# Kernel tuning notes

Measured on AMD Instinct MI355X. Metric: run time of the kernel, lower is better.

## Reference

```python
import jax, jax.numpy as jnp
import numpy as np

N, H, E, T = 100000, 128, 500000, 6  # nodes, hidden, max edges, edge types


def setup_inputs() -> dict:
    key = jax.random.key(0)
    ks = jax.random.split(key, 16)
    xav_e = float(np.sqrt(6.0 / (H + T * H)))  # xavier_uniform for edge_dense
    xav_h = float(np.sqrt(6.0 / (H + H)))
    u = lambda k, s, a: jax.random.uniform(k, s, jnp.float32, -a, a)
    return {
        "node_embeddings": jax.random.normal(ks[0], (N, H), jnp.float32),
        "W_edge": u(ks[1], (H, T * H), xav_e),
        "b_edge": 1e-6 * jax.random.normal(ks[2], (T * H,), jnp.float32),
        "W_ir": u(ks[3], (H, H), xav_h), "b_ir": jnp.zeros((H,), jnp.float32),
        "W_iz": u(ks[4], (H, H), xav_h), "b_iz": jnp.zeros((H,), jnp.float32),
        "W_in": u(ks[5], (H, H), xav_h), "b_in": jnp.zeros((H,), jnp.float32),
        "W_hr": u(ks[6], (H, H), xav_h),
        "W_hz": u(ks[7], (H, H), xav_h),
        "W_hn": u(ks[8], (H, H), xav_h), "b_hn": jnp.zeros((H,), jnp.float32),
        "source_indices": jax.random.randint(ks[9], (E,), 0, N, jnp.int32),
        "dest_indices": jax.random.randint(ks[10], (E,), 0, N, jnp.int32),
        "edge_types": jax.random.randint(ks[11], (E,), 0, T, jnp.int32),
        "num_edges": 450000,
    }


def reference(node_embeddings, W_edge, b_edge, W_ir, b_ir, W_iz, b_iz,
              W_in, b_in, W_hr, W_hz, W_hn, b_hn,
              source_indices, dest_indices, edge_types, num_edges):
    num_nodes, hidden = node_embeddings.shape
    max_edges = edge_types.shape[0]
    # gather source nodes, project to all edge types at once: [E, T*H]
    src = node_embeddings[source_indices]
    all_types = (src @ W_edge + b_edge).reshape(max_edges, -1, hidden)  # [E,T,H]
    # select per-edge type
    msg = jnp.take_along_axis(all_types, edge_types[:, None, None], axis=1)[:, 0, :]
    # mask padding edges, scatter-add into destination nodes
    msg = jnp.where((jnp.arange(max_edges) < num_edges)[:, None], msg, 0)
    agg = jax.ops.segment_sum(msg, dest_indices, num_segments=num_nodes)
    # GRU update: carry h = aggregated messages, inputs x = node_embeddings
    h, x = agg, node_embeddings
    r = jax.nn.sigmoid(x @ W_ir + b_ir + h @ W_hr)
    z = jax.nn.sigmoid(x @ W_iz + b_iz + h @ W_hz)
    n = jnp.tanh(x @ W_in + b_in + r * (h @ W_hn + b_hn))
    return (1.0 - z) * n + z * h
```

## Files before the change

### kernel.cpp

```cpp
#include <hip/hip_runtime.h>
#include <hip/hip_bf16.h>

#define HD 128
#define NT 6

typedef unsigned short u16;
typedef unsigned int u32;
typedef __attribute__((ext_vector_type(8))) short bf16x8;
typedef __attribute__((ext_vector_type(4))) float f32x4;

__device__ __forceinline__ float sigmoidf_(float x) {
  return 1.0f / (1.0f + __expf(-x));
}

__device__ __forceinline__ u16 f2bf(float x) {
  u32 u = __float_as_uint(x);
  return (u16)((u + 0x7FFFu + ((u >> 16) & 1u)) >> 16);
}
__device__ __forceinline__ float bflo(u32 v) { return __uint_as_float(v << 16); }
__device__ __forceinline__ float bfhi(u32 v) { return __uint_as_float(v & 0xffff0000u); }

__device__ __forceinline__ int swz(int p) { return p ^ (((p >> 8) & 7) << 4); }

__global__ void k_cvt_w(const float* __restrict__ We,
                        const float* __restrict__ Wir, const float* __restrict__ Wiz,
                        const float* __restrict__ Win, const float* __restrict__ Whr,
                        const float* __restrict__ Whz, const float* __restrict__ Whn,
                        u16* __restrict__ WeT, u16* __restrict__ WgT) {
  int i = blockIdx.x * blockDim.x + threadIdx.x;
  if (i < NT * HD * HD) {
    int c = i >> 7, k = i & 127;
    WeT[i] = f2bf(We[(size_t)k * (NT * HD) + c]);
  } else {
    int j = i - NT * HD * HD;
    if (j < 6 * HD * HD) {
      int m = j >> 14, jj = j & 16383;
      int c = jj >> 7, k = jj & 127;
      const float* W = (m == 0) ? Wir : (m == 1) ? Wiz : (m == 2) ? Win
                     : (m == 3) ? Whr : (m == 4) ? Whz : Whn;
      WgT[j] = f2bf(W[(size_t)k * HD + c]);
    }
  }
}

__global__ __launch_bounds__(256) void k_gemm_edge6(
    const float* __restrict__ X, const u16* __restrict__ WeT,
    const float* __restrict__ Be, u16* __restrict__ P, int N)
{
  __shared__ char As[32768];
  __shared__ char Bs[32768];
  const int tid = threadIdx.x;
  const int row0 = blockIdx.x * 128;

  #pragma unroll
  for (int i = 0; i < 8; ++i) {
    int p = i * 4096 + tid * 16;
    int row = row0 + (p >> 8);
    union { u16 u[8]; bf16x8 v; } ra;
    if (row < N) {
      const float4* s = (const float4*)(X + (size_t)row0 * HD + (p >> 1));
      float4 f0 = s[0], f1 = s[1];
      ra.u[0] = f2bf(f0.x); ra.u[1] = f2bf(f0.y); ra.u[2] = f2bf(f0.z); ra.u[3] = f2bf(f0.w);
      ra.u[4] = f2bf(f1.x); ra.u[5] = f2bf(f1.y); ra.u[6] = f2bf(f1.z); ra.u[7] = f2bf(f1.w);
    } else {
      #pragma unroll
      for (int j = 0; j < 8; ++j) ra.u[j] = 0;
    }
    *(bf16x8*)(As + swz(p)) = ra.v;
  }

  const int l = tid & 63, w = tid >> 6;
  const int m0 = (w >> 1) * 64, n0 = (w & 1) * 64;
  const int lr = l & 15, lg = l >> 4;
  f32x4 zero = {0.f, 0.f, 0.f, 0.f};

  for (int t = 0; t < NT; ++t) {
    __syncthreads();
    const char* gB = (const char*)(WeT + (size_t)t * HD * HD);
    #pragma unroll
    for (int i = 0; i < 8; ++i) {
      int p = i * 4096 + tid * 16;
      *(bf16x8*)(Bs + swz(p)) = *(const bf16x8*)(gB + p);
    }
    __syncthreads();

    f32x4 acc[4][4];
    #pragma unroll
    for (int m = 0; m < 4; ++m)
      #pragma unroll
      for (int n = 0; n < 4; ++n) acc[m][n] = zero;

    #pragma unroll
    for (int k = 0; k < 4; ++k) {
      bf16x8 a[4], b[4];
      #pragma unroll
      for (int m = 0; m < 4; ++m)
        a[m] = *(const bf16x8*)(As + swz((m0 + m * 16 + lr) * 256 + k * 64 + lg * 16));
      #pragma unroll
      for (int n = 0; n < 4; ++n)
        b[n] = *(const bf16x8*)(Bs + swz((n0 + n * 16 + lr) * 256 + k * 64 + lg * 16));
      #pragma unroll
      for (int m = 0; m < 4; ++m)
        #pragma unroll
        for (int n = 0; n < 4; ++n)
          acc[m][n] = __builtin_amdgcn_mfma_f32_16x16x32_bf16(a[m], b[n], acc[m][n], 0, 0, 0);
    }

    float bias[4];
    #pragma unroll
    for (int n = 0; n < 4; ++n) bias[n] = Be[t * HD + n0 + n * 16 + lr];
    #pragma unroll
    for (int m = 0; m < 4; ++m) {
      int rbase = row0 + m0 + m * 16 + lg * 4;
      #pragma unroll
      for (int j = 0; j < 4; ++j) {
        int row = rbase + j;
        if (row < N) {
          #pragma unroll
          for (int n = 0; n < 4; ++n)
            P[(size_t)row * (NT * HD) + t * HD + n0 + n * 16 + lr] =
                f2bf(acc[m][n][j] + bias[n]);
        }
      }
    }
  }
}

__global__ __launch_bounds__(256) void k_count(const int* __restrict__ dst,
                                               const int* __restrict__ nePtr,
                                               int* __restrict__ deg) {
  const int ne = nePtr[0];
  for (int e = blockIdx.x * blockDim.x + threadIdx.x; e < ne;
       e += gridDim.x * blockDim.x)
    atomicAdd(&deg[dst[e]], 1);
}

__global__ __launch_bounds__(256) void k_scan_a(const int* __restrict__ deg,
                                                int* __restrict__ off,
                                                int* __restrict__ bsum, int N) {
  __shared__ int s[256];
  const int b = blockIdx.x, tid = threadIdx.x;
  const int base = b * 1024 + tid * 4;
  int v0 = 0, v1 = 0, v2 = 0, v3 = 0;
  if (base < N) v0 = deg[base];
  if (base + 1 < N) v1 = deg[base + 1];
  if (base + 2 < N) v2 = deg[base + 2];
  if (base + 3 < N) v3 = deg[base + 3];
  const int sum = v0 + v1 + v2 + v3;
  s[tid] = sum;
  __syncthreads();
  for (int d = 1; d < 256; d <<= 1) {
    int t = (tid >= d) ? s[tid - d] : 0;
    __syncthreads();
    s[tid] += t;
    __syncthreads();
  }
  const int excl = s[tid] - sum;
  if (base < N) off[base] = excl;
  if (base + 1 < N) off[base + 1] = excl + v0;
  if (base + 2 < N) off[base + 2] = excl + v0 + v1;
  if (base + 3 < N) off[base + 3] = excl + v0 + v1 + v2;
  if (tid == 255) bsum[b] = s[255];
}

__global__ void k_scan_b(int* __restrict__ bsum, int nb) {
  __shared__ int s[1024];
  const int tid = threadIdx.x;
  const int v = (tid < nb) ? bsum[tid] : 0;
  s[tid] = v;
  __syncthreads();
  for (int d = 1; d < 1024; d <<= 1) {
    int t = (tid >= d) ? s[tid - d] : 0;
    __syncthreads();
    s[tid] += t;
    __syncthreads();
  }
  if (tid < nb) bsum[tid] = s[tid] - v;
}

__global__ __launch_bounds__(256) void k_scan_c(int* __restrict__ off,
                                                const int* __restrict__ bsum, int N) {
  const int b = blockIdx.x, tid = threadIdx.x;
  const int add = bsum[b];
  const int base = b * 1024 + tid * 4;
  #pragma unroll
  for (int i = 0; i < 4; ++i)
    if (base + i < N) off[base + i] += add;
}

__global__ __launch_bounds__(256) void k_fill(const int* __restrict__ src,
                                              const int* __restrict__ dst,
                                              const int* __restrict__ typ,
                                              const int* __restrict__ nePtr,
                                              int* __restrict__ off,
                                              u32* __restrict__ elist) {
  const int ne = nePtr[0];
  for (int e = blockIdx.x * blockDim.x + threadIdx.x; e < ne;
       e += gridDim.x * blockDim.x) {
    int pos = atomicAdd(&off[dst[e]], 1);
    elist[pos] = (u32)(src[e] * NT + typ[e]);
  }
}

__global__ __launch_bounds__(256) void k_gather(
    const u16* __restrict__ P, const int* __restrict__ deg,
    const int* __restrict__ off, const u32* __restrict__ elist,
    u16* __restrict__ Hb, int N)
{
  const int l = threadIdx.x & 63;
  int wid = (int)((blockIdx.x * blockDim.x + threadIdx.x) >> 6);
  int nw = (int)((gridDim.x * blockDim.x) >> 6);
  for (int n = wid; n < N; n += nw) {
    const int e1 = off[n];
    const int e0 = e1 - deg[n];
    float a0 = 0.f, a1 = 0.f, b0 = 0.f, b1 = 0.f;
    for (int e = e0; e < e1; e += 4) {
      u32 p0 = elist[e];
      u32 p1 = (e + 1 < e1) ? elist[e + 1] : p0;
      u32 p2 = (e + 2 < e1) ? elist[e + 2] : p0;
      u32 p3 = (e + 3 < e1) ? elist[e + 3] : p0;
      u32 v0 = *((const u32*)(P + (size_t)p0 * HD) + l);
      u32 v1 = *((const u32*)(P + (size_t)p1 * HD) + l);
      u32 v2 = *((const u32*)(P + (size_t)p2 * HD) + l);
      u32 v3 = *((const u32*)(P + (size_t)p3 * HD) + l);
      if (e + 1 >= e1) v1 = 0;
      if (e + 2 >= e1) v2 = 0;
      if (e + 3 >= e1) v3 = 0;
      a0 += bflo(v0); a1 += bfhi(v0);
      b0 += bflo(v1); b1 += bfhi(v1);
      a0 += bflo(v2); a1 += bfhi(v2);
      b0 += bflo(v3); b1 += bfhi(v3);
    }
    a0 += b0; a1 += b1;
    u32 hp = ((u32)f2bf(a1) << 16) | (u32)f2bf(a0);
    *((u32*)(Hb + (size_t)n * HD) + l) = hp;
  }
}

__global__ __launch_bounds__(256) void k_gru2(
    const float* __restrict__ X, const u16* __restrict__ Hb,
    const u16* __restrict__ WgT,
    const float* __restrict__ bir, const float* __restrict__ biz,
    const float* __restrict__ bin_, const float* __restrict__ bhn,
    float* __restrict__ out, int N)
{
  __shared__ char Xs[16384];
  __shared__ char Hs[16384];
  __shared__ char Wb[32768];
  const int tid = threadIdx.x;
  const int row0 = blockIdx.x * 64;

  #pragma unroll
  for (int i = 0; i < 4; ++i) {
    int p = i * 4096 + tid * 16;
    int row = row0 + (p >> 8);
    union { u16 u[8]; bf16x8 v; } rx, rh;
    if (row < N) {
      const float4* sx = (const float4*)(X + (size_t)row0 * HD + (p >> 1));
      float4 x0 = sx[0], x1 = sx[1];
      rx.u[0] = f2bf(x0.x); rx.u[1] = f2bf(x0.y); rx.u[2] = f2bf(x0.z); rx.u[3] = f2bf(x0.w);
      rx.u[4] = f2bf(x1.x); rx.u[5] = f2bf(x1.y); rx.u[6] = f2bf(x1.z); rx.u[7] = f2bf(x1.w);
      rh.v = *(const bf16x8*)((const char*)Hb + (size_t)row0 * 256 + p);
    } else {
      #pragma unroll
      for (int j = 0; j < 8; ++j) { rx.u[j] = 0; rh.u[j] = 0; }
    }
    *(bf16x8*)(Xs + swz(p)) = rx.v;
    *(bf16x8*)(Hs + swz(p)) = rh.v;
  }

  const int l = tid & 63, w = tid >> 6;
  const int lr = l & 15, lg = l >> 4;
  const int rloc = w * 16;

  auto stageW = [&](const u16* WT) {
    const char* g = (const char*)WT;
    #pragma unroll
    for (int i = 0; i < 8; ++i) {
      int p = i * 4096 + tid * 16;
      *(bf16x8*)(Wb + swz(p)) = *(const bf16x8*)(g + p);
    }
  };

  f32x4 zero = {0.f, 0.f, 0.f, 0.f};
  auto sweepL = [&](const char* Ab, f32x4* acc) {
    #pragma unroll
    for (int n = 0; n < 8; ++n) acc[n] = zero;
    #pragma unroll
    for (int k = 0; k < 4; ++k) {
      bf16x8 a = *(const bf16x8*)(Ab + swz((rloc + lr) * 256 + k * 64 + lg * 16));
      #pragma unroll
      for (int n = 0; n < 8; ++n) {
        bf16x8 b = *(const bf16x8*)(Wb + swz((n * 16 + lr) * 256 + k * 64 + lg * 16));
        acc[n] = __builtin_amdgcn_mfma_f32_16x16x32_bf16(a, b, acc[n], 0, 0, 0);
      }
    }
  };

  f32x4 t1[8], t2[8], rg[8], nn[8];
  float bv[8];

  __syncthreads(); stageW(WgT + 0 * HD * HD); __syncthreads();
  sweepL(Xs, t1);
  __syncthreads(); stageW(WgT + 3 * HD * HD); __syncthreads();
  sweepL(Hs, t2);
  #pragma unroll
  for (int n = 0; n < 8; ++n) bv[n] = bir[n * 16 + lr];
  #pragma unroll
  for (int n = 0; n < 8; ++n)
    #pragma unroll
    for (int j = 0; j < 4; ++j) rg[n][j] = sigmoidf_(t1[n][j] + bv[n] + t2[n][j]);

  __syncthreads(); stageW(WgT + 5 * HD * HD); __syncthreads();
  sweepL(Hs, t2);
  #pragma unroll
  for (int n = 0; n < 8; ++n) bv[n] = bhn[n * 16 + lr];
  #pragma unroll
  for (int n = 0; n < 8; ++n)
    #pragma unroll
    for (int j = 0; j < 4; ++j) rg[n][j] *= (t2[n][j] + bv[n]);

  __syncthreads(); stageW(WgT + 2 * HD * HD); __syncthreads();
  sweepL(Xs, t1);
  #pragma unroll
  for (int n = 0; n < 8; ++n) bv[n] = bin_[n * 16 + lr];
  #pragma unroll
  for (int n = 0; n < 8; ++n)
    #pragma unroll
    for (int j = 0; j < 4; ++j) nn[n][j] = tanhf(t1[n][j] + bv[n] + rg[n][j]);

  __syncthreads(); stageW(WgT + 1 * HD * HD); __syncthreads();
  sweepL(Xs, t1);
  __syncthreads(); stageW(WgT + 4 * HD * HD); __syncthreads();
  sweepL(Hs, t2);
  #pragma unroll
  for (int n = 0; n < 8; ++n) bv[n] = biz[n * 16 + lr];
  #pragma unroll
  for (int n = 0; n < 8; ++n) {
    #pragma unroll
    for (int j = 0; j < 4; ++j) {
      int row = row0 + rloc + lg * 4 + j;
      if (row < N) {
        float z = sigmoidf_(t1[n][j] + bv[n] + t2[n][j]);
        u16 hu = *(const u16*)(Hs + swz((rloc + lg * 4 + j) * 256 + (n * 16 + lr) * 2));
        float h = __uint_as_float((u32)hu << 16);
        out[(size_t)row * HD + n * 16 + lr] = (1.0f - z) * nn[n][j] + z * h;
      }
    }
  }
}

__global__ __launch_bounds__(256) void k_gather_gru(
    const float* __restrict__ X, const u16* __restrict__ P,
    const int* __restrict__ deg, const int* __restrict__ off,
    const u32* __restrict__ elist, const u16* __restrict__ WgT,
    const float* __restrict__ bir, const float* __restrict__ biz,
    const float* __restrict__ bin_, const float* __restrict__ bhn,
    float* __restrict__ out, int N)
{
  __shared__ char Xs[16384];
  __shared__ char Hs[16384];
  const int tid = threadIdx.x;
  const int l = tid & 63, w = tid >> 6;
  const int row0 = blockIdx.x * 64;
  const int wr0 = w * 16;

  #pragma unroll
  for (int it = 0; it < 4; ++it) {
    int chunk = it * 64 + l;
    int r = chunk >> 4, seg = chunk & 15;
    int grow = row0 + wr0 + r;
    union { u16 u[8]; bf16x8 v; } rx;
    if (grow < N) {
      const float4* sx = (const float4*)(X + (size_t)grow * HD + seg * 8);
      float4 x0 = sx[0], x1 = sx[1];
      rx.u[0] = f2bf(x0.x); rx.u[1] = f2bf(x0.y); rx.u[2] = f2bf(x0.z); rx.u[3] = f2bf(x0.w);
      rx.u[4] = f2bf(x1.x); rx.u[5] = f2bf(x1.y); rx.u[6] = f2bf(x1.z); rx.u[7] = f2bf(x1.w);
    } else {
      #pragma unroll
      for (int j = 0; j < 8; ++j) rx.u[j] = 0;
    }
    *(bf16x8*)(Xs + swz((wr0 + r) * 256 + seg * 16)) = rx.v;
  }

  for (int i = 0; i < 16; ++i) {
    int n = row0 + wr0 + i;
    float a0 = 0.f, a1 = 0.f;
    if (n < N) {
      int e1 = off[n];
      for (int e = e1 - deg[n]; e < e1; e += 4) {
        u32 p0 = elist[e];
        u32 p1 = (e + 1 < e1) ? elist[e + 1] : p0;
        u32 p2 = (e + 2 < e1) ? elist[e + 2] : p0;
        u32 p3 = (e + 3 < e1) ? elist[e + 3] : p0;
        u32 v0 = *((const u32*)(P + (size_t)p0 * HD) + l);
        u32 v1 = *((const u32*)(P + (size_t)p1 * HD) + l);
        u32 v2 = *((const u32*)(P + (size_t)p2 * HD) + l);
        u32 v3 = *((const u32*)(P + (size_t)p3 * HD) + l);
        if (e + 1 >= e1) v1 = 0;
        if (e + 2 >= e1) v2 = 0;
        if (e + 3 >= e1) v3 = 0;
        a0 += bflo(v0) + bflo(v1) + bflo(v2) + bflo(v3);
        a1 += bfhi(v0) + bfhi(v1) + bfhi(v2) + bfhi(v3);
      }
    }
    u32 hp = ((u32)f2bf(a1) << 16) | (u32)f2bf(a0);
    *(u32*)(Hs + swz((wr0 + i) * 256 + l * 4)) = hp;
  }

  const int lr = l & 15, lg = l >> 4;
  const int rloc = wr0;

  f32x4 zero = {0.f, 0.f, 0.f, 0.f};
  auto sweep = [&](const char* Ab, const u16* WT, f32x4* acc) {
    #pragma unroll
    for (int n = 0; n < 8; ++n) acc[n] = zero;
    #pragma unroll
    for (int k = 0; k < 4; ++k) {
      bf16x8 a = *(const bf16x8*)(Ab + swz((rloc + lr) * 256 + k * 64 + lg * 16));
      #pragma unroll
      for (int n = 0; n < 8; ++n) {
        bf16x8 b = *(const bf16x8*)(WT + (size_t)(n * 16 + lr) * HD + k * 32 + lg * 8);
        acc[n] = __builtin_amdgcn_mfma_f32_16x16x32_bf16(a, b, acc[n], 0, 0, 0);
      }
    }
  };

  f32x4 t1[8], t2[8], rg[8], nn[8];
  float bv[8];

  sweep(Xs, WgT + 0 * HD * HD, t1);
  sweep(Hs, WgT + 3 * HD * HD, t2);
  #pragma unroll
  for (int n = 0; n < 8; ++n) bv[n] = bir[n * 16 + lr];
  #pragma unroll
  for (int n = 0; n < 8; ++n)
    #pragma unroll
    for (int j = 0; j < 4; ++j) rg[n][j] = sigmoidf_(t1[n][j] + bv[n] + t2[n][j]);

  sweep(Hs, WgT + 5 * HD * HD, t2);
  #pragma unroll
  for (int n = 0; n < 8; ++n) bv[n] = bhn[n * 16 + lr];
  #pragma unroll
  for (int n = 0; n < 8; ++n)
    #pragma unroll
    for (int j = 0; j < 4; ++j) rg[n][j] *= (t2[n][j] + bv[n]);

  sweep(Xs, WgT + 2 * HD * HD, t1);
  #pragma unroll
  for (int n = 0; n < 8; ++n) bv[n] = bin_[n * 16 + lr];
  #pragma unroll
  for (int n = 0; n < 8; ++n)
    #pragma unroll
    for (int j = 0; j < 4; ++j) nn[n][j] = tanhf(t1[n][j] + bv[n] + rg[n][j]);

  sweep(Xs, WgT + 1 * HD * HD, t1);
  sweep(Hs, WgT + 4 * HD * HD, t2);
  #pragma unroll
  for (int n = 0; n < 8; ++n) bv[n] = biz[n * 16 + lr];
  #pragma unroll
  for (int n = 0; n < 8; ++n) {
    #pragma unroll
    for (int j = 0; j < 4; ++j) {
      int row = row0 + rloc + lg * 4 + j;
      if (row < N) {
        float z = sigmoidf_(t1[n][j] + bv[n] + t2[n][j]);
        u16 hu = *(const u16*)(Hs + swz((rloc + lg * 4 + j) * 256 + (n * 16 + lr) * 2));
        float h = __uint_as_float((u32)hu << 16);
        out[(size_t)row * HD + n * 16 + lr] = (1.0f - z) * nn[n][j] + z * h;
      }
    }
  }
}

__global__ __launch_bounds__(256) void k_scatter(
    const u16* __restrict__ P, const int* __restrict__ src,
    const int* __restrict__ dst, const int* __restrict__ typ,
    const int* __restrict__ nePtr, float* __restrict__ agg,
    int ldP, int fixedType)
{
  const int ne = nePtr[0];
  const int lane = threadIdx.x & 63;
  const int wid = (int)((blockIdx.x * blockDim.x + threadIdx.x) >> 6);
  const int nw = (int)((gridDim.x * blockDim.x) >> 6);
  for (int e = wid; e < ne; e += nw) {
    const int t = typ[e];
    if (fixedType >= 0 && t != fixedType) continue;
    const size_t po = (ldP == HD) ? (size_t)src[e] * HD
                                  : (size_t)src[e] * (NT * HD) + (size_t)t * HD;
    u32 v = *(const u32*)(P + po + lane * 2);
    float* o = agg + (size_t)dst[e] * HD + lane * 2;
    unsafeAtomicAdd(o, bflo(v));
    unsafeAtomicAdd(o + 1, bfhi(v));
  }
}

__global__ __launch_bounds__(256) void k_gru(
    const float* __restrict__ X, const float* __restrict__ agg,
    const u16* __restrict__ WgT,
    const float* __restrict__ bir, const float* __restrict__ biz,
    const float* __restrict__ bin_, const float* __restrict__ bhn,
    float* __restrict__ out, int N)
{
  __shared__ char Xs[16384];
  __shared__ char Hs[16384];
  const int tid = threadIdx.x;
  const int row0 = blockIdx.x * 64;

  #pragma unroll
  for (int i = 0; i < 4; ++i) {
    int p = i * 4096 + tid * 16;
    int row = row0 + (p >> 8);
    union { u16 u[8]; bf16x8 v; } rx, rh;
    if (row < N) {
      const float4* sx = (const float4*)(X + (size_t)row0 * HD + (p >> 1));
      const float4* sh = (const float4*)(agg + (size_t)row0 * HD + (p >> 1));
      float4 x0 = sx[0], x1 = sx[1], h0 = sh[0], h1 = sh[1];
      rx.u[0] = f2bf(x0.x); rx.u[1] = f2bf(x0.y); rx.u[2] = f2bf(x0.z); rx.u[3] = f2bf(x0.w);
      rx.u[4] = f2bf(x1.x); rx.u[5] = f2bf(x1.y); rx.u[6] = f2bf(x1.z); rx.u[7] = f2bf(x1.w);
      rh.u[0] = f2bf(h0.x); rh.u[1] = f2bf(h0.y); rh.u[2] = f2bf(h0.z); rh.u[3] = f2bf(h0.w);
      rh.u[4] = f2bf(h1.x); rh.u[5] = f2bf(h1.y); rh.u[6] = f2bf(h1.z); rh.u[7] = f2bf(h1.w);
    } else {
      #pragma unroll
      for (int j = 0; j < 8; ++j) { rx.u[j] = 0; rh.u[j] = 0; }
    }
    *(bf16x8*)(Xs + swz(p)) = rx.v;
    *(bf16x8*)(Hs + swz(p)) = rh.v;
  }
  __syncthreads();

  const int l = tid & 63, w = tid >> 6;
  const int lr = l & 15, lg = l >> 4;
  const int rloc = w * 16;

  f32x4 zero = {0.f, 0.f, 0.f, 0.f};
  auto sweep = [&](const char* Ab, const u16* WT, f32x4* acc) {
    #pragma unroll
    for (int n = 0; n < 8; ++n) acc[n] = zero;
    #pragma unroll
    for (int k = 0; k < 4; ++k) {
      bf16x8 a = *(const bf16x8*)(Ab + swz((rloc + lr) * 256 + k * 64 + lg * 16));
      #pragma unroll
      for (int n = 0; n < 8; ++n) {
        bf16x8 b = *(const bf16x8*)(WT + (size_t)(n * 16 + lr) * HD + k * 32 + lg * 8);
        acc[n] = __builtin_amdgcn_mfma_f32_16x16x32_bf16(a, b, acc[n], 0, 0, 0);
      }
    }
  };

  f32x4 t1[8], t2[8], rg[8], nn[8];
  float bv[8];

  sweep(Xs, WgT + 0 * HD * HD, t1);
  sweep(Hs, WgT + 3 * HD * HD, t2);
  #pragma unroll
  for (int n = 0; n < 8; ++n) bv[n] = bir[n * 16 + lr];
  #pragma unroll
  for (int n = 0; n < 8; ++n)
    #pragma unroll
    for (int j = 0; j < 4; ++j) rg[n][j] = sigmoidf_(t1[n][j] + bv[n] + t2[n][j]);

  sweep(Hs, WgT + 5 * HD * HD, t2);
  #pragma unroll
  for (int n = 0; n < 8; ++n) bv[n] = bhn[n * 16 + lr];
  #pragma unroll
  for (int n = 0; n < 8; ++n)
    #pragma unroll
    for (int j = 0; j < 4; ++j) rg[n][j] *= (t2[n][j] + bv[n]);

  sweep(Xs, WgT + 2 * HD * HD, t1);
  #pragma unroll
  for (int n = 0; n < 8; ++n) bv[n] = bin_[n * 16 + lr];
  #pragma unroll
  for (int n = 0; n < 8; ++n)
    #pragma unroll
    for (int j = 0; j < 4; ++j) nn[n][j] = tanhf(t1[n][j] + bv[n] + rg[n][j]);

  sweep(Xs, WgT + 1 * HD * HD, t1);
  sweep(Hs, WgT + 4 * HD * HD, t2);
  #pragma unroll
  for (int n = 0; n < 8; ++n) bv[n] = biz[n * 16 + lr];
  #pragma unroll
  for (int n = 0; n < 8; ++n) {
    #pragma unroll
    for (int j = 0; j < 4; ++j) {
      int row = row0 + rloc + lg * 4 + j;
      if (row < N) {
        float z = sigmoidf_(t1[n][j] + bv[n] + t2[n][j]);
        float h = agg[(size_t)row * HD + n * 16 + lr];
        out[(size_t)row * HD + n * 16 + lr] = (1.0f - z) * nn[n][j] + z * h;
      }
    }
  }
}

extern "C" void kernel_launch(void* const* d_in, const int* in_sizes, int n_in,
                              void* d_out, int out_size, void* d_ws, size_t ws_size,
                              hipStream_t stream) {
  const float* X      = (const float*)d_in[0];
  const float* W_edge = (const float*)d_in[1];
  const float* b_edge = (const float*)d_in[2];
  const float* b_ir   = (const float*)d_in[4];
  const float* b_iz   = (const float*)d_in[6];
  const float* b_in   = (const float*)d_in[8];
  const float* b_hn   = (const float*)d_in[12];
  const int* src      = (const int*)d_in[13];
  const int* dst      = (const int*)d_in[14];
  const int* typ      = (const int*)d_in[15];
  const int* nePtr    = (const int*)d_in[16];

  const int N = in_sizes[0] / HD;
  const int E = in_sizes[13];
  char* ws = (char*)d_ws;

  size_t cur = 0;
  auto alloc = [&](size_t bytes) {
    size_t p = cur;
    cur = (cur + bytes + 255) & ~(size_t)255;
    return p;
  };
  u16* WeT   = (u16*)(ws + alloc((size_t)NT * HD * HD * 2));
  u16* WgT   = (u16*)(ws + alloc((size_t)6 * HD * HD * 2));
  int* deg   = (int*)(ws + alloc((size_t)N * 4));
  int* offA  = (int*)(ws + alloc((size_t)N * 4));
  int* bsum  = (int*)(ws + alloc(1024 * 4));
  u32* elist = (u32*)(ws + alloc((size_t)E * 4));
  size_t base_need = cur;
  u16* P     = (u16*)(ws + alloc((size_t)N * NT * HD * 2));
  const size_t csr_need = cur;
  u16* Hb    = (u16*)(ws + alloc((size_t)N * HD * 2));
  const size_t split_need = cur;

  const int gb = (N + 127) / 128;
  const int NB = (N + 1023) / 1024;

  k_cvt_w<<<(NT * HD * HD + 6 * HD * HD + 255) / 256, 256, 0, stream>>>(
      W_edge, (const float*)d_in[3], (const float*)d_in[5], (const float*)d_in[7],
      (const float*)d_in[9], (const float*)d_in[10], (const float*)d_in[11], WeT, WgT);

  if (ws_size >= csr_need) {
    hipMemsetAsync(deg, 0, (size_t)N * 4, stream);
    k_gemm_edge6<<<gb, 256, 0, stream>>>(X, WeT, b_edge, P, N);
    k_count<<<1024, 256, 0, stream>>>(dst, nePtr, deg);
    k_scan_a<<<NB, 256, 0, stream>>>(deg, offA, bsum, N);
    k_scan_b<<<1, 1024, 0, stream>>>(bsum, NB);
    k_scan_c<<<NB, 256, 0, stream>>>(offA, bsum, N);
    k_fill<<<1024, 256, 0, stream>>>(src, dst, typ, nePtr, offA, elist);
    if (ws_size >= split_need) {
      k_gather<<<(N + 3) / 4, 256, 0, stream>>>(P, deg, offA, elist, Hb, N);
      k_gru2<<<(N + 63) / 64, 256, 0, stream>>>(
          X, Hb, WgT, b_ir, b_iz, b_in, b_hn, (float*)d_out, N);
    } else {
      k_gather_gru<<<(N + 63) / 64, 256, 0, stream>>>(
          X, P, deg, offA, elist, WgT, b_ir, b_iz, b_in, b_hn, (float*)d_out, N);
    }
  } else {
    float* agg = (float*)d_out;
    hipMemsetAsync(d_out, 0, (size_t)out_size * sizeof(float), stream);
    size_t pneed = base_need + (size_t)N * NT * HD * 2;
    if (ws_size >= pneed) {
      u16* Pf = (u16*)(ws + base_need);
      k_gemm_edge6<<<gb, 256, 0, stream>>>(X, WeT, b_edge, Pf, N);
      k_scatter<<<2048, 256, 0, stream>>>(Pf, src, dst, typ, nePtr, agg, NT * HD, -1);
      k_gru<<<(N + 63) / 64, 256, 0, stream>>>(X, agg, WgT, b_ir, b_iz, b_in, b_hn, agg, N);
    }
  }
}
```

Measured before the change: 275.0 us.

## Double-buffer GRU weight staging with register prefetch and larger row tiles

Replaces the GRU kernel with a 512-thread, 128-row-per-block version that double-buffers the six weight matrices in shared memory. Each next weight matrix is loaded into registers while the current sweep runs, which halves the barriers per stage and overlaps global loads with MFMA work. The final h value is now re-read from global memory instead of LDS. Shared memory use grows to 128KB per block, which limits occupancy to one block per CU despite the launch bound hint.

```diff
diff --git a/kernel.cpp b/kernel.cpp
--- a/kernel.cpp
+++ b/kernel.cpp
@@ -237,22 +237,25 @@
   }
 }
 
-__global__ __launch_bounds__(256) void k_gru2(
+__global__ __launch_bounds__(512, 2) void k_gru3(
     const float* __restrict__ X, const u16* __restrict__ Hb,
     const u16* __restrict__ WgT,
     const float* __restrict__ bir, const float* __restrict__ biz,
     const float* __restrict__ bin_, const float* __restrict__ bhn,
     float* __restrict__ out, int N)
 {
-  __shared__ char Xs[16384];
-  __shared__ char Hs[16384];
-  __shared__ char Wb[32768];
+  __shared__ char Xs[32768];
+  __shared__ char Hs[32768];
+  __shared__ char Wb[2][32768];
   const int tid = threadIdx.x;
-  const int row0 = blockIdx.x * 64;
+  const int row0 = blockIdx.x * 128;
+  const int l = tid & 63, w = tid >> 6;
+  const int lr = l & 15, lg = l >> 4;
+  const int rloc = w * 16;
 
   #pragma unroll
   for (int i = 0; i < 4; ++i) {
-    int p = i * 4096 + tid * 16;
+    int p = i * 8192 + tid * 16;
     int row = row0 + (p >> 8);
     union { u16 u[8]; bf16x8 v; } rx, rh;
     if (row < N) {
@@ -269,21 +272,23 @@
     *(bf16x8*)(Hs + swz(p)) = rh.v;
   }
 
-  const int l = tid & 63, w = tid >> 6;
-  const int lr = l & 15, lg = l >> 4;
-  const int rloc = w * 16;
-
-  auto stageW = [&](const u16* WT) {
-    const char* g = (const char*)WT;
-    #pragma unroll
-    for (int i = 0; i < 8; ++i) {
-      int p = i * 4096 + tid * 16;
-      *(bf16x8*)(Wb + swz(p)) = *(const bf16x8*)(g + p);
-    }
+  bf16x8 wreg[4];
+  auto loadW = [&](int g) {
+    const char* gp = (const char*)(WgT + (size_t)g * HD * HD);
+    #pragma unroll
+    for (int i = 0; i < 4; ++i)
+      wreg[i] = *(const bf16x8*)(gp + i * 8192 + tid * 16);
   };
+  auto writeW = [&](int buf) {
+    #pragma unroll
+    for (int i = 0; i < 4; ++i) {
+      int p = i * 8192 + tid * 16;
+      *(bf16x8*)(Wb[buf] + swz(p)) = wreg[i];
+    }
+  };
 
   f32x4 zero = {0.f, 0.f, 0.f, 0.f};
-  auto sweepL = [&](const char* Ab, f32x4* acc) {
+  auto sweepL = [&](const char* Ab, const char* Wp, f32x4* acc) {
     #pragma unroll
     for (int n = 0; n < 8; ++n) acc[n] = zero;
     #pragma unroll
@@ -291,7 +296,7 @@
       bf16x8 a = *(const bf16x8*)(Ab + swz((rloc + lr) * 256 + k * 64 + lg * 16));
       #pragma unroll
       for (int n = 0; n < 8; ++n) {
-        bf16x8 b = *(const bf16x8*)(Wb + swz((n * 16 + lr) * 256 + k * 64 + lg * 16));
+        bf16x8 b = *(const bf16x8*)(Wp + swz((n * 16 + lr) * 256 + k * 64 + lg * 16));
         acc[n] = __builtin_amdgcn_mfma_f32_16x16x32_bf16(a, b, acc[n], 0, 0, 0);
       }
     }
@@ -300,39 +305,53 @@
   f32x4 t1[8], t2[8], rg[8], nn[8];
   float bv[8];
 
-  __syncthreads(); stageW(WgT + 0 * HD * HD); __syncthreads();
-  sweepL(Xs, t1);
-  __syncthreads(); stageW(WgT + 3 * HD * HD); __syncthreads();
-  sweepL(Hs, t2);
+  loadW(0); writeW(0);
+  __syncthreads();
+
+  loadW(3);
+  sweepL(Xs, Wb[0], t1);
+  writeW(1);
+  __syncthreads();
+
+  loadW(5);
+  sweepL(Hs, Wb[1], t2);
+  writeW(0);
   #pragma unroll
   for (int n = 0; n < 8; ++n) bv[n] = bir[n * 16 + lr];
   #pragma unroll
   for (int n = 0; n < 8; ++n)
     #pragma unroll
     for (int j = 0; j < 4; ++j) rg[n][j] = sigmoidf_(t1[n][j] + bv[n] + t2[n][j]);
-
-  __syncthreads(); stageW(WgT + 5 * HD * HD); __syncthreads();
-  sweepL(Hs, t2);
+  __syncthreads();
+
+  loadW(2);
+  sweepL(Hs, Wb[0], t2);
+  writeW(1);
   #pragma unroll
   for (int n = 0; n < 8; ++n) bv[n] = bhn[n * 16 + lr];
   #pragma unroll
   for (int n = 0; n < 8; ++n)
     #pragma unroll
     for (int j = 0; j < 4; ++j) rg[n][j] *= (t2[n][j] + bv[n]);
-
-  __syncthreads(); stageW(WgT + 2 * HD * HD); __syncthreads();
-  sweepL(Xs, t1);
+  __syncthreads();
+
+  loadW(1);
+  sweepL(Xs, Wb[1], t1);
+  writeW(0);
   #pragma unroll
   for (int n = 0; n < 8; ++n) bv[n] = bin_[n * 16 + lr];
   #pragma unroll
   for (int n = 0; n < 8; ++n)
     #pragma unroll
     for (int j = 0; j < 4; ++j) nn[n][j] = tanhf(t1[n][j] + bv[n] + rg[n][j]);
-
-  __syncthreads(); stageW(WgT + 1 * HD * HD); __syncthreads();
-  sweepL(Xs, t1);
-  __syncthreads(); stageW(WgT + 4 * HD * HD); __syncthreads();
-  sweepL(Hs, t2);
+  __syncthreads();
+
+  loadW(4);
+  sweepL(Xs, Wb[0], t1);
+  writeW(1);
+  __syncthreads();
+
+  sweepL(Hs, Wb[1], t2);
   #pragma unroll
   for (int n = 0; n < 8; ++n) bv[n] = biz[n * 16 + lr];
   #pragma unroll
@@ -341,10 +360,11 @@
     for (int j = 0; j < 4; ++j) {
       int row = row0 + rloc + lg * 4 + j;
       if (row < N) {
+        int col = n * 16 + lr;
         float z = sigmoidf_(t1[n][j] + bv[n] + t2[n][j]);
-        u16 hu = *(const u16*)(Hs + swz((rloc + lg * 4 + j) * 256 + (n * 16 + lr) * 2));
+        u16 hu = Hb[(size_t)row * HD + col];
         float h = __uint_as_float((u32)hu << 16);
-        out[(size_t)row * HD + n * 16 + lr] = (1.0f - z) * nn[n][j] + z * h;
+        out[(size_t)row * HD + col] = (1.0f - z) * nn[n][j] + z * h;
       }
     }
   }
@@ -648,7 +668,7 @@
     k_fill<<<1024, 256, 0, stream>>>(src, dst, typ, nePtr, offA, elist);
     if (ws_size >= split_need) {
       k_gather<<<(N + 3) / 4, 256, 0, stream>>>(P, deg, offA, elist, Hb, N);
-      k_gru2<<<(N + 63) / 64, 256, 0, stream>>>(
+      k_gru3<<<gb, 512, 0, stream>>>(
           X, Hb, WgT, b_ir, b_iz, b_in, b_hn, (float*)d_out, N);
     } else {
       k_gather_gru<<<(N + 63) / 64, 256, 0, stream>>>(
```

Result: faster. 253.6 us (-7.8%).
